# Optimization experiments

Measured on AMD Instinct MI355X. Metric: run time of the kernel, lower is better.

Reference implementation:

```python
import jax, jax.numpy as jnp
import numpy as np

# dims
B, A, CIN, CC = 512, 256, 7, 16          # batch, num_actions, input channels, conv channels
D, H, DH, E = 48, 8, 6, 512              # token_dimension, heads, head_dim, num_embeddings
S, T = 32, 32                            # num_input_tokens, num_output_tokens
AH = H * DH                              # 48
NL = 4                                   # attention layers
CONV_IN = A * CC                         # 4096
ENC = S * D                              # 1536
DEC_OUT = A * CIN                        # 1792
SCALE = float(np.sqrt(D))                # module uses sqrt(input_embedding_dim)
EPS = 1e-5


def _ln(x, g, b):
    m = jnp.mean(x, axis=-1, keepdims=True)
    v = jnp.var(x, axis=-1, keepdims=True)
    return (x - m) * jax.lax.rsqrt(v + EPS) * g + b


def setup_inputs() -> dict:
    key = jax.random.key(0)
    ks = iter(jax.random.split(key, 64))
    def rn(shape, s=0.05):
        return jax.random.normal(next(ks), shape, dtype=jnp.float32) * s
    inp = {}
    inp['x'] = jax.random.normal(next(ks), (B, A, CIN), dtype=jnp.float32)
    inp['u'] = jax.random.uniform(next(ks), (T, B), dtype=jnp.float32)
    inp['bn_g'] = jnp.ones((CIN,), jnp.float32); inp['bn_b'] = jnp.zeros((CIN,), jnp.float32)
    inp['conv_w'] = rn((CC, CIN, 5)); inp['conv_b'] = jnp.zeros((CC,), jnp.float32)
    inp['tk_W1'] = rn((CONV_IN, 2 * CONV_IN)); inp['tk_b1'] = jnp.zeros((2 * CONV_IN,), jnp.float32)
    inp['tk_W2'] = rn((2 * CONV_IN, ENC)); inp['tk_b2'] = jnp.zeros((ENC,), jnp.float32)
    for nm in ('q', 'k', 'v'):
        inp['ln%s_g' % nm] = jnp.ones((NL, D), jnp.float32)
        inp['ln%s_b' % nm] = jnp.zeros((NL, D), jnp.float32)
        inp['W%s' % nm] = rn((NL, D, AH))
        inp['b%s' % nm] = jnp.zeros((NL, AH), jnp.float32)
    inp['Wo'] = rn((NL, AH, D)); inp['bo'] = jnp.zeros((NL, D), jnp.float32)
    inp['mln_g'] = jnp.ones((NL, D), jnp.float32); inp['mln_b'] = jnp.zeros((NL, D), jnp.float32)
    inp['W1'] = rn((NL, D, 2 * D)); inp['b1'] = jnp.zeros((NL, 2 * D), jnp.float32)
    inp['W2'] = rn((NL, 2 * D, D)); inp['b2'] = jnp.zeros((NL, D), jnp.float32)
    inp['emb'] = rn((D, E), 1.0)          # nn.Parameter(torch.randn(D, E))
    inp['pos_enc'] = rn((T, D), 1.0)      # nn.Parameter(torch.randn(T, D))
    inp['dec_W1'] = rn((ENC, 2 * ENC)); inp['dec_b1'] = jnp.zeros((2 * ENC,), jnp.float32)
    inp['dec_W2'] = rn((2 * ENC, DEC_OUT)); inp['dec_b2'] = jnp.zeros((DEC_OUT,), jnp.float32)
    return inp


def _fwd(x, u, bn_g, bn_b, conv_w, conv_b, tk_W1, tk_b1, tk_W2, tk_b2,
         lnq_g, lnq_b, Wq, bq, lnk_g, lnk_b, Wk, bk, lnv_g, lnv_b, Wv, bv, Wo, bo,
         mln_g, mln_b, W1, b1, W2, b2, emb, pos_enc, dec_W1, dec_b1, dec_W2, dec_b2):
    # --- conv stem (BatchNorm1d in training mode: batch statistics) ---
    xt = x.transpose(0, 2, 1)                              # [B, 7, A]
    mu = jnp.mean(xt, axis=(0, 2), keepdims=True)
    var = jnp.var(xt, axis=(0, 2), keepdims=True)
    xn = (xt - mu) * jax.lax.rsqrt(var + EPS) * bn_g[None, :, None] + bn_b[None, :, None]
    xc = jax.lax.conv_general_dilated(xn, conv_w, (1,), ((2, 2),),
                                      dimension_numbers=('NCH', 'OIH', 'NCH')) + conv_b[None, :, None]
    xf = xc.reshape(B, -1)                                 # [B, 16*A]
    h = jax.nn.relu(xf @ tk_W1 + tk_b1)
    toks = (h @ tk_W2 + tk_b2).reshape(B, S, D)            # [B, S, D]

    STOT = S + T
    kc = jnp.zeros((NL, B, H, STOT, DH), jnp.float32)
    vc = jnp.zeros_like(kc)

    # --- prefill pass (output discarded; fills KV caches) ---
    ii = jnp.arange(S)[:, None]; jj = jnp.arange(S)[None, :]
    pre_mask = jnp.where(jj - ii >= S - 1, -999.0, 0.0)    # triu(-999, diagonal=S-1), as in source
    xcur = toks
    for l in range(NL):
        q = (_ln(xcur, lnq_g[l], lnq_b[l]) @ Wq[l] + bq[l]).reshape(B, S, H, DH).transpose(0, 2, 1, 3)
        k = (_ln(xcur, lnk_g[l], lnk_b[l]) @ Wk[l] + bk[l]).reshape(B, S, H, DH).transpose(0, 2, 1, 3)
        v = (_ln(xcur, lnv_g[l], lnv_b[l]) @ Wv[l] + bv[l]).reshape(B, S, H, DH).transpose(0, 2, 1, 3)
        kc = kc.at[l, :, :, :S].set(k)
        vc = vc.at[l, :, :, :S].set(v)
        attn = jax.nn.softmax(jnp.einsum('bhqd,bhkd->bhqk', q, k) / SCALE + pre_mask, axis=-1)
        o = jnp.einsum('bhqk,bhkd->bhqd', attn, v).transpose(0, 2, 1, 3).reshape(B, S, AH)
        xcur = o @ Wo[l] + bo[l] + xcur
        hh = jax.nn.relu(_ln(xcur, mln_g[l], mln_b[l]) @ W1[l] + b1[l])
        xcur = hh @ W2[l] + b2[l]

    jidx = jnp.arange(STOT)

    def step(carry, xs):
        kc, vc = carry
        i, pe, uu = xs
        p = S + i                                          # cache length before this step
        xtk = jnp.broadcast_to(pe, (B, 1, D))
        newk, newv = [], []
        for l in range(NL):
            q = (_ln(xtk, lnq_g[l], lnq_b[l]) @ Wq[l] + bq[l]).reshape(B, 1, H, DH).transpose(0, 2, 1, 3)
            k = (_ln(xtk, lnk_g[l], lnk_b[l]) @ Wk[l] + bk[l]).reshape(B, 1, H, DH).transpose(0, 2, 1, 3)
            v = (_ln(xtk, lnv_g[l], lnv_b[l]) @ Wv[l] + bv[l]).reshape(B, 1, H, DH).transpose(0, 2, 1, 3)
            kcl = jax.lax.dynamic_update_slice(kc[l], k, (0, 0, p, 0))
            vcl = jax.lax.dynamic_update_slice(vc[l], v, (0, 0, p, 0))
            scores = jnp.einsum('bhqd,bhkd->bhqk', q, kcl) / SCALE
            # source mask: -999 added for positions >= mask_offset (includes the new token itself)
            scores = scores + jnp.where(jidx >= p, -999.0, 0.0)
            attn = jax.nn.softmax(scores, axis=-1)
            o = jnp.einsum('bhqk,bhkd->bhqd', attn, vcl).transpose(0, 2, 1, 3).reshape(B, 1, AH)
            xtk = o @ Wo[l] + bo[l] + xtk
            hh = jax.nn.relu(_ln(xtk, mln_g[l], mln_b[l]) @ W1[l] + b1[l])
            xtk = hh @ W2[l] + b2[l]
            newk.append(kcl); newv.append(vcl)
        attended = xtk                                     # [B, 1, D]
        probs = jax.nn.softmax((attended @ emb).reshape(B, E), axis=1)
        cdf = jnp.cumsum(probs, axis=1)
        idx = jnp.clip(jnp.sum((cdf < uu[:, None]).astype(jnp.int32), axis=1), 0, E - 1)
        sel = emb.T[idx].reshape(B, 1, D)
        st = sel + attended - jax.lax.stop_gradient(attended)  # straight-through
        return (jnp.stack(newk), jnp.stack(newv)), st

    (_, _), outs = jax.lax.scan(step, (kc, vc), (jnp.arange(T), pos_enc, u))
    out_tokens = outs.transpose(1, 0, 2, 3).reshape(B, T * D)
    dh_ = jax.nn.relu(out_tokens @ dec_W1 + dec_b1)
    traj = (dh_ @ dec_W2 + dec_b2).reshape(B, A, CIN)
    return traj


def reference(x, u, bn_g, bn_b, conv_w, conv_b, tk_W1, tk_b1, tk_W2, tk_b2,
              lnq_g, lnq_b, Wq, bq, lnk_g, lnk_b, Wk, bk, lnv_g, lnv_b, Wv, bv, Wo, bo,
              mln_g, mln_b, W1, b1, W2, b2, emb, pos_enc, dec_W1, dec_b1, dec_W2, dec_b2):
    return _fwd(x, u, bn_g, bn_b, conv_w, conv_b, tk_W1, tk_b1, tk_W2, tk_b2,
                lnq_g, lnq_b, Wq, bq, lnk_g, lnk_b, Wk, bk, lnv_g, lnv_b, Wv, bv, Wo, bo,
                mln_g, mln_b, W1, b1, W2, b2, emb, pos_enc, dec_W1, dec_b1, dec_W2, dec_b2)
```

## Files before the change

### kernel.cpp

```cpp
#include <hip/hip_runtime.h>

static const double SCALE_ = 6.928203230275509;

__device__ inline float  fma_t(float a, float b, float c)  { return fmaf(a, b, c); }
__device__ inline double fma_t(double a, double b, double c){ return fma(a, b, c); }

__device__ __attribute__((noinline)) double dotW(const double* a,
                                                 const float* W, int n, int ldw,
                                                 double init) {
  double a0 = init, a1 = 0.0;
#pragma unroll 2
  for (int i = 0; i < n; i += 2) {
    a0 = fma(a[i],     (double)W[i * ldw],       a0);
    a1 = fma(a[i + 1], (double)W[(i + 1) * ldw], a1);
  }
  return a0 + a1;
}

template <int N, typename WP>
__device__ __forceinline__ double dotN(const double* a, WP W, int ldw, double init) {
  double c0 = init, c1 = 0.0, c2 = 0.0, c3 = 0.0;
#pragma unroll
  for (int i = 0; i < N; i += 4) {
    c0 = fma(a[i],     (double)W[i * ldw],       c0);
    c1 = fma(a[i + 1], (double)W[(i + 1) * ldw], c1);
    c2 = fma(a[i + 2], (double)W[(i + 2) * ldw], c2);
    c3 = fma(a[i + 3], (double)W[(i + 3) * ldw], c3);
  }
  return (c0 + c1) + (c2 + c3);
}

__device__ __forceinline__ double dot48_row(const double* a, const float* Wrow, double init) {
  double c0 = init, c1 = 0.0, c2 = 0.0, c3 = 0.0;
#pragma unroll
  for (int i = 0; i < 48; i += 4) {
    const float4 wv = *(const float4*)(Wrow + i);
    c0 = fma(a[i],     (double)wv.x, c0);
    c1 = fma(a[i + 1], (double)wv.y, c1);
    c2 = fma(a[i + 2], (double)wv.z, c2);
    c3 = fma(a[i + 3], (double)wv.w, c3);
  }
  return (c0 + c1) + (c2 + c3);
}

__device__ __forceinline__ double dot96_row(const double* a, const float* Wrow, double init) {
  double c0 = init, c1 = 0.0, c2 = 0.0, c3 = 0.0;
#pragma unroll
  for (int i = 0; i < 96; i += 4) {
    const float4 wv = *(const float4*)(Wrow + i);
    c0 = fma(a[i],     (double)wv.x, c0);
    c1 = fma(a[i + 1], (double)wv.y, c1);
    c2 = fma(a[i + 2], (double)wv.z, c2);
    c3 = fma(a[i + 3], (double)wv.w, c3);
  }
  return (c0 + c1) + (c2 + c3);
}

__device__ __attribute__((noinline)) double2 ln_stats48(const double* x) {
  double s0 = 0, s1 = 0, q0 = 0, q1 = 0;
#pragma unroll 2
  for (int i = 0; i < 48; i += 2) {
    const double va = x[i], vb = x[i + 1];
    s0 += va; q0 = fma(va, va, q0);
    s1 += vb; q1 = fma(vb, vb, q1);
  }
  const double m = (s0 + s1) / 48.0;
  const double rs = 1.0 / sqrt((q0 + q1) / 48.0 - m * m + 1e-5);
  return make_double2(m, rs);
}

__device__ __attribute__((noinline)) double exp_ni(double x) { return exp(x); }

__global__ __launch_bounds__(256) void bn_partial_kernel(const float* __restrict__ x,
                                                         double* __restrict__ part) {
  __shared__ double sh[256 * 14];
  const int tid = threadIdx.x;
  const int idx = blockIdx.x * 256 + tid;
  const float* p = x + (size_t)idx * 7;
  for (int c = 0; c < 7; ++c) {
    double v = (double)p[c];
    sh[tid * 14 + c] = v;
    sh[tid * 14 + 7 + c] = v * v;
  }
  __syncthreads();
  if (tid < 14) {
    double acc = 0.0;
    for (int t = 0; t < 256; ++t) acc += sh[t * 14 + tid];
    part[blockIdx.x * 14 + tid] = acc;
  }
}

__global__ void bn_final_kernel(const double* __restrict__ part,
                                const float* __restrict__ g, const float* __restrict__ bb,
                                double* __restrict__ stat) {
  const int c = threadIdx.x;
  if (c < 7) {
    double s = 0.0, s2 = 0.0;
    for (int i = 0; i < 512; ++i) { s += part[i * 14 + c]; s2 += part[i * 14 + 7 + c]; }
    const double mean = s / 131072.0;
    const double var = s2 / 131072.0 - mean * mean;
    const double rstd = 1.0 / sqrt(var + 1e-5);
    const double scale = rstd * (double)g[c];
    stat[c] = scale;
    stat[7 + c] = (double)bb[c] - mean * scale;
  }
}

__global__ __launch_bounds__(256) void conv_kernel(const float* __restrict__ x,
                                                   const float* __restrict__ wconv,
                                                   const float* __restrict__ cb,
                                                   const double* __restrict__ stat,
                                                   double* __restrict__ xf) {
  __shared__ double wsh[560 + 14];
  const int tid = threadIdx.x;
  for (int i = tid; i < 560; i += 256) wsh[i] = (double)wconv[i];
  for (int i = tid; i < 14; i += 256) wsh[560 + i] = stat[i];
  __syncthreads();
  const int idx = blockIdx.x * 256 + tid;
  const int a = idx & 255;
  const int o = (idx >> 8) & 15;
  const int b = idx >> 12;
  double acc = (double)cb[o];
  const float* xb = x + (size_t)b * (256 * 7);
  for (int k = 0; k < 5; ++k) {
    const int pos = a + k - 2;
    if (pos < 0 || pos >= 256) continue;
    const float* xp = xb + pos * 7;
    for (int ci = 0; ci < 7; ++ci) {
      const double xn = (double)xp[ci] * wsh[560 + ci] + wsh[567 + ci];
      acc = fma(xn, wsh[(o * 7 + ci) * 5 + k], acc);
    }
  }
  xf[idx] = acc;
}

template <typename T, bool BIAS, bool RELU>
__global__ __launch_bounds__(256) void gemm128_kernel(const T* __restrict__ A,
                                                      const float* __restrict__ Bm,
                                                      const float* __restrict__ bias,
                                                      T* __restrict__ C,
                                                      const int M, const int N, const int K,
                                                      const int kc) {
  __shared__ T As[16][130];
  __shared__ T Bs[16][66];
  const int tid = threadIdx.x;
  const int tx = tid & 15, ty = tid >> 4;
  const int n0 = blockIdx.x * 64, m0 = blockIdx.y * 128;
  const int k0 = blockIdx.z * kc, kend = k0 + kc;
  const int ar = tid >> 1, ac = (tid & 1) * 8;
  const int br = tid >> 4, bc = (tid & 15) * 4;
  const T* Ap = A + (size_t)(m0 + ar) * K;
  const float* Bp = Bm + (size_t)br * N + n0 + bc;
  T acc[8][4] = {};
  for (int k = k0; k < kend; k += 16) {
    T av8[8];
#pragma unroll
    for (int i = 0; i < 8; ++i) av8[i] = Ap[k + ac + i];
    const float4 bw = *(const float4*)(Bp + (size_t)k * N);
#pragma unroll
    for (int i = 0; i < 8; ++i) As[ac + i][ar] = av8[i];
    Bs[br][bc] = (T)bw.x; Bs[br][bc + 1] = (T)bw.y;
    Bs[br][bc + 2] = (T)bw.z; Bs[br][bc + 3] = (T)bw.w;
    __syncthreads();
#pragma unroll
    for (int kk = 0; kk < 16; ++kk) {
      T a[8], b[4];
#pragma unroll
      for (int i = 0; i < 8; ++i) a[i] = As[kk][ty * 8 + i];
#pragma unroll
      for (int j = 0; j < 4; ++j) b[j] = Bs[kk][tx * 4 + j];
#pragma unroll
      for (int i = 0; i < 8; ++i)
#pragma unroll
        for (int j = 0; j < 4; ++j) acc[i][j] = fma_t(a[i], b[j], acc[i][j]);
    }
    __syncthreads();
  }
  T* Cp = C + (size_t)blockIdx.z * M * N;
#pragma unroll
  for (int i = 0; i < 8; ++i) {
    const int row = m0 + ty * 8 + i;
#pragma unroll
    for (int j = 0; j < 4; ++j) {
      const int col = n0 + tx * 4 + j;
      T v = acc[i][j];
      if (BIAS) v += (T)bias[col];
      if (RELU) v = v > (T)0 ? v : (T)0;
      Cp[(size_t)row * N + col] = v;
    }
  }
}

template <typename T, bool BIAS, bool RELU>
__global__ __launch_bounds__(256) void gemm_kernel(const T* __restrict__ A,
                                                   const float* __restrict__ Bm,
                                                   const float* __restrict__ bias,
                                                   T* __restrict__ C,
                                                   const int M, const int N, const int K,
                                                   const int kc) {
  __shared__ T As[16][65];
  __shared__ T Bs[16][65];
  const int tid = threadIdx.x;
  const int tx = tid & 15, ty = tid >> 4;
  const int n0 = blockIdx.x * 64, m0 = blockIdx.y * 64;
  const int k0 = blockIdx.z * kc, kend = k0 + kc;
  const int ar = tid >> 2, ac = (tid & 3) * 4;
  const int br = tid >> 4, bc = (tid & 15) * 4;
  const T* Ap = A + (size_t)(m0 + ar) * K;
  const float* Bp = Bm + (size_t)br * N + n0 + bc;
  T acc[4][4] = {};
  for (int k = k0; k < kend; k += 16) {
    const T a0 = Ap[k + ac], a1 = Ap[k + ac + 1], a2 = Ap[k + ac + 2], a3 = Ap[k + ac + 3];
    const float4 bw = *(const float4*)(Bp + (size_t)k * N);
    As[ac][ar] = a0; As[ac + 1][ar] = a1; As[ac + 2][ar] = a2; As[ac + 3][ar] = a3;
    Bs[br][bc] = (T)bw.x; Bs[br][bc + 1] = (T)bw.y; Bs[br][bc + 2] = (T)bw.z; Bs[br][bc + 3] = (T)bw.w;
    __syncthreads();
#pragma unroll
    for (int kk = 0; kk < 16; ++kk) {
      T av[4], bv2[4];
#pragma unroll
      for (int i = 0; i < 4; ++i) av[i] = As[kk][ty * 4 + i];
#pragma unroll
      for (int j = 0; j < 4; ++j) bv2[j] = Bs[kk][tx * 4 + j];
#pragma unroll
      for (int i = 0; i < 4; ++i)
#pragma unroll
        for (int j = 0; j < 4; ++j) acc[i][j] = fma_t(av[i], bv2[j], acc[i][j]);
    }
    __syncthreads();
  }
  T* Cp = C + (size_t)blockIdx.z * M * N;
#pragma unroll
  for (int i = 0; i < 4; ++i) {
    const int row = m0 + ty * 4 + i;
#pragma unroll
    for (int j = 0; j < 4; ++j) {
      const int col = n0 + tx * 4 + j;
      T v = acc[i][j];
      if (BIAS) v += (T)bias[col];
      if (RELU) v = v > (T)0 ? v : (T)0;
      Cp[(size_t)row * N + col] = v;
    }
  }
}

__global__ __launch_bounds__(256) void reduce2_bias_kernel(const double* __restrict__ part,
                                                           const float* __restrict__ bias,
                                                           double* __restrict__ out,
                                                           const int MN, const int N) {
  const int i = blockIdx.x * 256 + threadIdx.x;
  if (i < MN) out[i] = part[i] + part[MN + i] + (double)bias[i % N];
}

__global__ __launch_bounds__(256) void transpose_weights_kernel(
    const float* __restrict__ Wq, const float* __restrict__ Wk,
    const float* __restrict__ Wv, const float* __restrict__ Wo,
    const float* __restrict__ W1, const float* __restrict__ W2,
    const float* __restrict__ emb,
    float* __restrict__ WqT, float* __restrict__ WkT,
    float* __restrict__ WvT, float* __restrict__ WoT,
    float* __restrict__ W1T, float* __restrict__ W2T,
    float* __restrict__ embT) {
  const int t = blockIdx.x * 256 + threadIdx.x;
  if (t < 36864) {
    const int a = t / 9216, r = t - a * 9216;
    const int l = r / 2304, e = r - l * 2304;
    const int i = e / 48, j = e - i * 48;
    const float* src = a == 0 ? Wq : a == 1 ? Wk : a == 2 ? Wv : Wo;
    float* dst = a == 0 ? WqT : a == 1 ? WkT : a == 2 ? WvT : WoT;
    dst[l * 2304 + j * 48 + i] = src[l * 2304 + i * 48 + j];
  } else if (t < 55296) {
    const int t1 = t - 36864;
    const int l = t1 / 4608, e = t1 - l * 4608;
    const int i = e / 96, j = e - i * 96;
    W1T[l * 4608 + j * 48 + i] = W1[l * 4608 + i * 96 + j];
  } else if (t < 73728) {
    const int t2 = t - 55296;
    const int l = t2 / 4608, e = t2 - l * 4608;
    const int i = e / 48, j = e - i * 48;
    W2T[l * 4608 + j * 96 + i] = W2[l * 4608 + i * 48 + j];
  } else {
    const int t3 = t - 73728;
    const int d = t3 / 512, e = t3 - d * 512;
    embT[e * 48 + d] = emb[d * 512 + e];
  }
}

__global__ __launch_bounds__(256) void prefill_kernel(
    const double* __restrict__ toks,
    const float* __restrict__ lnq_g, const float* __restrict__ lnq_b,
    const float* __restrict__ Wq, const float* __restrict__ bq,
    const float* __restrict__ lnk_g, const float* __restrict__ lnk_b,
    const float* __restrict__ Wk, const float* __restrict__ bk,
    const float* __restrict__ lnv_g, const float* __restrict__ lnv_b,
    const float* __restrict__ Wv, const float* __restrict__ bvv,
    const float* __restrict__ Wo, const float* __restrict__ bo,
    const float* __restrict__ mln_g, const float* __restrict__ mln_b,
    const float* __restrict__ W1, const float* __restrict__ b1,
    const float* __restrict__ W2, const float* __restrict__ b2,
    float* __restrict__ kc32, float* __restrict__ vc32) {
  const int b = blockIdx.x, tid = threadIdx.x;
  __shared__ double xcur[1536], abuf[1536], qbuf[1536], kvbuf[3072];
  __shared__ double mean[32], rstd[32];
  double* kb = kvbuf;
  double* vb = kvbuf + 1536;

#pragma unroll 1
  for (int i = tid; i < 1536; i += 256) xcur[i] = toks[(size_t)b * 1536 + i];
  __syncthreads();

#pragma unroll 1
  for (int l = 0; l < 4; ++l) {
    if (tid < 32) {
      double s = 0.0, s2 = 0.0;
#pragma unroll 4
      for (int i = 0; i < 48; ++i) { const double v = xcur[tid * 48 + i]; s += v; s2 += v * v; }
      const double m = s / 48.0;
      mean[tid] = m;
      rstd[tid] = 1.0 / sqrt(s2 / 48.0 - m * m + 1e-5);
    }
    __syncthreads();
    const bool last = (l == 3);

    if (!last) {
#pragma unroll 1
      for (int i = tid; i < 1536; i += 256) {
        const int t = i / 48, d = i % 48;
        abuf[i] = (xcur[i] - mean[t]) * rstd[t] * (double)lnq_g[l * 48 + d] + (double)lnq_b[l * 48 + d];
      }
      __syncthreads();
#pragma unroll 1
      for (int i = tid; i < 1536; i += 256) {
        const int t = i / 48, j = i % 48;
        qbuf[i] = dotW(abuf + t * 48, Wq + l * 2304 + j, 48, 48, (double)bq[l * 48 + j]);
      }
      __syncthreads();
    }
#pragma unroll 1
    for (int i = tid; i < 1536; i += 256) {
      const int t = i / 48, d = i % 48;
      abuf[i] = (xcur[i] - mean[t]) * rstd[t] * (double)lnk_g[l * 48 + d] + (double)lnk_b[l * 48 + d];
    }
    __syncthreads();
#pragma unroll 1
    for (int i = tid; i < 1536; i += 256) {
      const int t = i / 48, j = i % 48;
      kb[i] = dotW(abuf + t * 48, Wk + l * 2304 + j, 48, 48, (double)bk[l * 48 + j]);
    }
    __syncthreads();
#pragma unroll 1
    for (int i = tid; i < 1536; i += 256) {
      const int t = i / 48, d = i % 48;
      abuf[i] = (xcur[i] - mean[t]) * rstd[t] * (double)lnv_g[l * 48 + d] + (double)lnv_b[l * 48 + d];
    }
    __syncthreads();
#pragma unroll 1
    for (int i = tid; i < 1536; i += 256) {
      const int t = i / 48, j = i % 48;
      vb[i] = dotW(abuf + t * 48, Wv + l * 2304 + j, 48, 48, (double)bvv[l * 48 + j]);
    }
    __syncthreads();
#pragma unroll 1
    for (int i = tid; i < 1536; i += 256) {
      const int t = i / 48, j = i % 48;
      const int h = j / 6, d = j % 6;
      const size_t ci = ((((size_t)b * 4 + l) * 8 + h) * 32 + t) * 6 + d;
      kc32[ci] = (float)kb[i];
      vc32[ci] = (float)vb[i];
    }

    if (!last) {
      const int t = tid >> 3, h = tid & 7;
      const double* qp = qbuf + t * 48 + h * 6;
      const double q0 = qp[0], q1 = qp[1], q2 = qp[2], q3 = qp[3], q4 = qp[4], q5 = qp[5];
      double mx = -1e300;
#pragma unroll 4
      for (int j = 0; j < 32; ++j) {
        const double* kp = kb + j * 48 + h * 6;
        double sv = q0 * kp[0];
        sv = fma(q1, kp[1], sv); sv = fma(q2, kp[2], sv); sv = fma(q3, kp[3], sv);
        sv = fma(q4, kp[4], sv); sv = fma(q5, kp[5], sv);
        sv /= SCALE_;
        if (t == 0 && j == 31) sv -= 999.0;
        mx = sv > mx ? sv : mx;
      }
      double den = 0, o0 = 0, o1 = 0, o2 = 0, o3 = 0, o4 = 0, o5 = 0;
#pragma unroll 4
      for (int j = 0; j < 32; ++j) {
        const double* kp = kb + j * 48 + h * 6;
        double sv = q0 * kp[0];
        sv = fma(q1, kp[1], sv); sv = fma(q2, kp[2], sv); sv = fma(q3, kp[3], sv);
        sv = fma(q4, kp[4], sv); sv = fma(q5, kp[5], sv);
        sv /= SCALE_;
        if (t == 0 && j == 31) sv -= 999.0;
        const double e = exp_ni(sv - mx);
        den += e;
        const double* vp = vb + j * 48 + h * 6;
        o0 = fma(e, vp[0], o0); o1 = fma(e, vp[1], o1); o2 = fma(e, vp[2], o2);
        o3 = fma(e, vp[3], o3); o4 = fma(e, vp[4], o4); o5 = fma(e, vp[5], o5);
      }
      abuf[t * 48 + h * 6 + 0] = o0 / den;
      abuf[t * 48 + h * 6 + 1] = o1 / den;
      abuf[t * 48 + h * 6 + 2] = o2 / den;
      abuf[t * 48 + h * 6 + 3] = o3 / den;
      abuf[t * 48 + h * 6 + 4] = o4 / den;
      abuf[t * 48 + h * 6 + 5] = o5 / den;
      __syncthreads();
#pragma unroll 1
      for (int i = tid; i < 1536; i += 256) {
        const int t2 = i / 48, j = i % 48;
        xcur[i] += dotW(abuf + t2 * 48, Wo + l * 2304 + j, 48, 48, (double)bo[l * 48 + j]);
      }
      __syncthreads();
      if (tid < 32) {
        double s = 0.0, s2 = 0.0;
#pragma unroll 4
        for (int i = 0; i < 48; ++i) { const double v = xcur[tid * 48 + i]; s += v; s2 += v * v; }
        const double m = s / 48.0;
        mean[tid] = m;
        rstd[tid] = 1.0 / sqrt(s2 / 48.0 - m * m + 1e-5);
      }
      __syncthreads();
#pragma unroll 1
      for (int i = tid; i < 1536; i += 256) {
        const int t2 = i / 48, d = i % 48;
        qbuf[i] = (xcur[i] - mean[t2]) * rstd[t2] * (double)mln_g[l * 48 + d] + (double)mln_b[l * 48 + d];
      }
      __syncthreads();
#pragma unroll 1
      for (int i = tid; i < 3072; i += 256) {
        const int t2 = i / 96, jj = i % 96;
        const double acc = dotW(qbuf + t2 * 48, W1 + l * 4608 + jj, 48, 96, (double)b1[l * 96 + jj]);
        kvbuf[i] = acc > 0 ? acc : 0;
      }
      __syncthreads();
#pragma unroll 1
      for (int i = tid; i < 1536; i += 256) {
        const int t2 = i / 48, j = i % 48;
        abuf[i] = dotW(kvbuf + t2 * 96, W2 + l * 4608 + j, 96, 48, (double)b2[l * 48 + j]);
      }
      __syncthreads();
#pragma unroll 1
      for (int i = tid; i < 1536; i += 256) xcur[i] = abuf[i];
      __syncthreads();
    }
  }
}

__global__ __launch_bounds__(256, 2) void ar_kernel(
    const float* __restrict__ pos_enc, const float* __restrict__ u,
    const float* __restrict__ lnq_g, const float* __restrict__ lnq_b,
    const float* __restrict__ WqT, const float* __restrict__ bq,
    const float* __restrict__ lnk_g, const float* __restrict__ lnk_b,
    const float* __restrict__ WkT, const float* __restrict__ bk,
    const float* __restrict__ lnv_g, const float* __restrict__ lnv_b,
    const float* __restrict__ WvT, const float* __restrict__ bvv,
    const float* __restrict__ WoT, const float* __restrict__ bo,
    const float* __restrict__ mln_g, const float* __restrict__ mln_b,
    const float* __restrict__ W1T, const float* __restrict__ b1,
    const float* __restrict__ W2T, const float* __restrict__ b2,
    const float* __restrict__ emb,
    const float* __restrict__ kc32, const float* __restrict__ vc32,
    float* __restrict__ out_tok) {
  const int b = blockIdx.x, tid = threadIdx.x;
  __shared__ float knew[4][8][32][7];
  __shared__ float vnew[4][8][32][7];
  __shared__ double xtk[48], anorm[144], qs[48], os[48], hh[96];
  __shared__ double probs[512], red[4];
  __shared__ float par[2880];
  {
    const float* srcs[14] = {lnq_g, lnq_b, lnk_g, lnk_b, lnv_g, lnv_b, mln_g, mln_b,
                             bq, bk, bvv, bo, b1, b2};
    const int sz[14] = {192, 192, 192, 192, 192, 192, 192, 192, 192, 192, 192, 192, 384, 192};
    int base = 0;
#pragma unroll 1
    for (int a2 = 0; a2 < 14; ++a2) {
      for (int i = tid; i < sz[a2]; i += 256) par[base + i] = srcs[a2][i];
      base += sz[a2];
    }
  }
  __syncthreads();

  const int hl = tid >> 5, rl = tid & 31;

#pragma unroll 1
  for (int step = 0; step < 32; ++step) {
    const int p = 32 + step;
    if (tid < 48) xtk[tid] = (double)pos_enc[step * 48 + tid];
    __syncthreads();

#pragma unroll 1
    for (int l = 0; l < 4; ++l) {
      {
        const double2 st = ln_stats48(xtk);
        if (tid < 144) {
          const int which = tid / 48, d = tid - which * 48;
          const float* gp = par + 384 * which;
          const float* bp = gp + 192;
          anorm[tid] = (xtk[d] - st.x) * st.y * (double)gp[l * 48 + d] + (double)bp[l * 48 + d];
        }
      }
      __syncthreads();
      if (tid < 144) {
        const int which = tid / 48, j = tid - which * 48;
        const float* WT = which == 0 ? WqT : which == 1 ? WkT : WvT;
        const float* bbp = par + 1536 + 192 * which;
        const double acc = dot48_row(anorm + which * 48, WT + l * 2304 + j * 48,
                                     (double)bbp[l * 48 + j]);
        if (which == 0) {
          qs[j] = acc;
        } else {
          const int h2 = j / 6, d2 = j - h2 * 6;
          if (which == 1) knew[l][h2][step][d2] = (float)acc;
          else            vnew[l][h2][step][d2] = (float)acc;
        }
      }
      __syncthreads();
      {
        const size_t gb = (((size_t)b * 4 + l) * 8 + hl) * 192 + rl * 6;
        const float* kg = kc32 + gb;
        const float* vg = vc32 + gb;
        const double qv0 = qs[hl * 6 + 0], qv1 = qs[hl * 6 + 1], qv2 = qs[hl * 6 + 2],
                     qv3 = qs[hl * 6 + 3], qv4 = qs[hl * 6 + 4], qv5 = qs[hl * 6 + 5];
        const bool has2 = rl < step;
        double sv1 = qv0 * (double)kg[0];
        sv1 = fma(qv1, (double)kg[1], sv1); sv1 = fma(qv2, (double)kg[2], sv1);
        sv1 = fma(qv3, (double)kg[3], sv1); sv1 = fma(qv4, (double)kg[4], sv1);
        sv1 = fma(qv5, (double)kg[5], sv1);
        sv1 /= SCALE_;
        double sv2 = -1e300;
        if (has2) {
          const float* kh = &knew[l][hl][rl][0];
          double t2 = qv0 * (double)kh[0];
          t2 = fma(qv1, (double)kh[1], t2); t2 = fma(qv2, (double)kh[2], t2);
          t2 = fma(qv3, (double)kh[3], t2); t2 = fma(qv4, (double)kh[4], t2);
          t2 = fma(qv5, (double)kh[5], t2);
          sv2 = t2 / SCALE_;
        }
        double mx = sv1 > sv2 ? sv1 : sv2;
#pragma unroll
        for (int off = 1; off < 32; off <<= 1) { const double o2 = __shfl_xor(mx, off); mx = o2 > mx ? o2 : mx; }
        const double e1 = exp(sv1 - mx);
        const double e2 = has2 ? exp(sv2 - mx) : 0.0;
        double den = e1 + e2;
        double o[6];
#pragma unroll
        for (int d = 0; d < 6; ++d) o[d] = e1 * (double)vg[d];
        if (has2) {
          const float* vh = &vnew[l][hl][rl][0];
#pragma unroll
          for (int d = 0; d < 6; ++d) o[d] = fma(e2, (double)vh[d], o[d]);
        }
#pragma unroll
        for (int off = 1; off < 32; off <<= 1) {
          den += __shfl_xor(den, off);
#pragma unroll
          for (int d = 0; d < 6; ++d) o[d] += __shfl_xor(o[d], off);
        }
        if (rl == 0) {
#pragma unroll
          for (int d = 0; d < 6; ++d) os[hl * 6 + d] = o[d] / den;
        }
      }
      __syncthreads();
      if (tid < 48)
        xtk[tid] += dot48_row(os, WoT + l * 2304 + tid * 48, (double)par[2112 + l * 48 + tid]);
      __syncthreads();
      {
        const double2 st = ln_stats48(xtk);
        if (tid < 48)
          anorm[tid] = (xtk[tid] - st.x) * st.y * (double)par[1152 + l * 48 + tid]
                       + (double)par[1344 + l * 48 + tid];
      }
      __syncthreads();
      if (tid < 96) {
        const double v2 = dot48_row(anorm, W1T + l * 4608 + tid * 48, (double)par[2304 + l * 96 + tid]);
        hh[tid] = v2 > 0 ? v2 : 0;
      }
      __syncthreads();
      if (tid < 48)
        xtk[tid] = dot96_row(hh, W2T + l * 4608 + tid * 96, (double)par[2688 + l * 48 + tid]);
      __syncthreads();
    }

    {
      const double lg1 = dotN<48>(xtk, emb + tid, 512, 0.0);
      const double lg2 = dotN<48>(xtk, emb + 256 + tid, 512, 0.0);
      double mx = lg1 > lg2 ? lg1 : lg2;
#pragma unroll
      for (int off = 1; off < 64; off <<= 1) { const double o2 = __shfl_xor(mx, off); mx = o2 > mx ? o2 : mx; }
      if ((tid & 63) == 0) red[tid >> 6] = mx;
      __syncthreads();
      {
        const double m0 = red[0] > red[1] ? red[0] : red[1];
        const double m1 = red[2] > red[3] ? red[2] : red[3];
        mx = m0 > m1 ? m0 : m1;
      }
      probs[tid] = exp(lg1 - mx);
      probs[tid + 256] = exp(lg2 - mx);
      __syncthreads();
      if (tid < 64) {
        const int lane = tid;
        double loc[8], run = 0;
#pragma unroll
        for (int n2 = 0; n2 < 8; ++n2) { run += probs[lane * 8 + n2]; loc[n2] = run; }
        double incl = run;
#pragma unroll
        for (int off = 1; off < 64; off <<= 1) {
          const double t2 = __shfl_up(incl, off);
          if (lane >= off) incl += t2;
        }
        const double excl = incl - run;
        const double Ssum = __shfl(incl, 63);
        const double uu = (double)u[step * 512 + b];
        int cnt = 0;
#pragma unroll
        for (int n2 = 0; n2 < 8; ++n2) cnt += ((excl + loc[n2]) / Ssum < uu) ? 1 : 0;
#pragma unroll
        for (int off = 1; off < 64; off <<= 1) cnt += __shfl_xor(cnt, off);
        const int idx = cnt > 511 ? 511 : cnt;
        if (lane < 48) {
          const double sel = (double)emb[lane * 512 + idx];
          const double att = xtk[lane];
          out_tok[(size_t)b * 1536 + step * 48 + lane] = (float)((sel + att) - att);
        }
      }
      __syncthreads();
    }
  }
}

extern "C" void kernel_launch(void* const* d_in, const int* in_sizes, int n_in,
                              void* d_out, int out_size, void* d_ws, size_t ws_size,
                              hipStream_t stream) {
  const float* x      = (const float*)d_in[0];
  const float* u      = (const float*)d_in[1];
  const float* bn_g   = (const float*)d_in[2];
  const float* bn_b   = (const float*)d_in[3];
  const float* conv_w = (const float*)d_in[4];
  const float* conv_b = (const float*)d_in[5];
  const float* tk_W1  = (const float*)d_in[6];
  const float* tk_b1  = (const float*)d_in[7];
  const float* tk_W2  = (const float*)d_in[8];
  const float* tk_b2  = (const float*)d_in[9];
  const float* lnq_g  = (const float*)d_in[10];
  const float* lnq_b  = (const float*)d_in[11];
  const float* Wq     = (const float*)d_in[12];
  const float* bq     = (const float*)d_in[13];
  const float* lnk_g  = (const float*)d_in[14];
  const float* lnk_b  = (const float*)d_in[15];
  const float* Wk     = (const float*)d_in[16];
  const float* bk     = (const float*)d_in[17];
  const float* lnv_g  = (const float*)d_in[18];
  const float* lnv_b  = (const float*)d_in[19];
  const float* Wv     = (const float*)d_in[20];
  const float* bvv    = (const float*)d_in[21];
  const float* Wo     = (const float*)d_in[22];
  const float* bo     = (const float*)d_in[23];
  const float* mln_g  = (const float*)d_in[24];
  const float* mln_b  = (const float*)d_in[25];
  const float* W1     = (const float*)d_in[26];
  const float* b1     = (const float*)d_in[27];
  const float* W2     = (const float*)d_in[28];
  const float* b2     = (const float*)d_in[29];
  const float* emb    = (const float*)d_in[30];
  const float* pos    = (const float*)d_in[31];
  const float* dW1    = (const float*)d_in[32];
  const float* db1    = (const float*)d_in[33];
  const float* dW2    = (const float*)d_in[34];
  const float* db2    = (const float*)d_in[35];
  float* out = (float*)d_out;

  char* w = (char*)d_ws;
  size_t off = 0;
  auto alloc = [&](size_t bytes) {
    size_t o = off;
    off = (off + bytes + 255) & ~(size_t)255;
    return o;
  };
  const size_t o_bnp  = alloc(512 * 14 * 8);
  const size_t o_bns  = alloc(14 * 8);
  const size_t o_xf   = alloc(16777216);
  const size_t o_h    = alloc(33554432);
  const size_t o_toks = alloc(6291456);
  const size_t o_kc   = alloc(12582912);
  const size_t o_vc   = alloc(12582912);

  double* bnp  = (double*)(w + o_bnp);
  double* bns  = (double*)(w + o_bns);
  double* xf   = (double*)(w + o_xf);
  double* hbuf = (double*)(w + o_h);
  double* toks = (double*)(w + o_toks);
  float*  kc32 = (float*)(w + o_kc);
  float*  vc32 = (float*)(w + o_vc);
  double* part = (double*)(w + o_xf);
  float*  otok = (float*)(w + o_h);
  float*  dh   = (float*)(w + o_h + 4194304);
  float* WqT  = (float*)(w + o_h + 16777216);
  float* WkT  = WqT + 9216;
  float* WvT  = WkT + 9216;
  float* WoT  = WvT + 9216;
  float* W1T  = WoT + 9216;
  float* W2T  = W1T + 18432;
  float* embT = W2T + 18432;

  bn_partial_kernel<<<512, 256, 0, stream>>>(x, bnp);
  bn_final_kernel<<<1, 64, 0, stream>>>(bnp, bn_g, bn_b, bns);
  conv_kernel<<<8192, 256, 0, stream>>>(x, conv_w, conv_b, bns, xf);
  gemm128_kernel<double, true, true><<<dim3(128, 4, 1), 256, 0, stream>>>(
      xf, tk_W1, tk_b1, hbuf, 512, 8192, 4096, 4096);
  gemm128_kernel<double, false, false><<<dim3(24, 4, 2), 256, 0, stream>>>(
      hbuf, tk_W2, nullptr, part, 512, 1536, 8192, 4096);
  reduce2_bias_kernel<<<3072, 256, 0, stream>>>(part, tk_b2, toks, 512 * 1536, 1536);
  transpose_weights_kernel<<<384, 256, 0, stream>>>(Wq, Wk, Wv, Wo, W1, W2, emb,
      WqT, WkT, WvT, WoT, W1T, W2T, embT);
  prefill_kernel<<<512, 256, 0, stream>>>(toks,
      lnq_g, lnq_b, Wq, bq, lnk_g, lnk_b, Wk, bk, lnv_g, lnv_b, Wv, bvv,
      Wo, bo, mln_g, mln_b, W1, b1, W2, b2, kc32, vc32);
  ar_kernel<<<512, 256, 0, stream>>>(pos, u,
      lnq_g, lnq_b, WqT, bq, lnk_g, lnk_b, WkT, bk, lnv_g, lnv_b, WvT, bvv,
      WoT, bo, mln_g, mln_b, W1T, b1, W2T, b2, emb, kc32, vc32, otok);
  gemm_kernel<float, true, true><<<dim3(48, 8, 1), 256, 0, stream>>>(
      otok, dW1, db1, dh, 512, 3072, 1536, 1536);
  gemm_kernel<float, true, false><<<dim3(28, 8, 1), 256, 0, stream>>>(
      dh, dW2, db2, out, 512, 1792, 3072, 3072);
}
```

Measured before the change: 4.462 ms.

## Prefetch weights into registers, fuse layernorm stats via wave shuffles, lighten barriers

The sequential decode kernel now loads the Q/K/V, Wo and W1 weight rows and the K/V cache values into registers before the barriers that precede their use. The idea is to overlap global load latency with earlier phases. Layernorm statistics are computed once per wave with shuffle reductions and broadcast through shared memory, replacing the per-thread serial ln_stats48 loops. This fuses the Wo projection, residual add and layernorm into one phase and removes a barrier. __syncthreads is replaced by a custom barrier that waits only on LDS counters, which relies on register-held global loads not needing a vmcnt wait and raises register pressure.

Result: slower. 4.803 ms (+7.6%).

```diff
diff --git a/kernel.cpp b/kernel.cpp
--- a/kernel.cpp
+++ b/kernel.cpp
@@ -4,6 +4,12 @@
 
 __device__ inline float  fma_t(float a, float b, float c)  { return fmaf(a, b, c); }
 __device__ inline double fma_t(double a, double b, double c){ return fma(a, b, c); }
+
+#define BARRIER() do {                                         \
+    asm volatile("s_waitcnt lgkmcnt(0)" ::: "memory");         \
+    __builtin_amdgcn_s_barrier();                              \
+    asm volatile("" ::: "memory");                             \
+  } while (0)
 
 __device__ __attribute__((noinline)) double dotW(const double* a,
                                                  const float* W, int n, int ldw,
@@ -54,19 +60,6 @@
     c3 = fma(a[i + 3], (double)wv.w, c3);
   }
   return (c0 + c1) + (c2 + c3);
-}
-
-__device__ __attribute__((noinline)) double2 ln_stats48(const double* x) {
-  double s0 = 0, s1 = 0, q0 = 0, q1 = 0;
-#pragma unroll 2
-  for (int i = 0; i < 48; i += 2) {
-    const double va = x[i], vb = x[i + 1];
-    s0 += va; q0 = fma(va, va, q0);
-    s1 += vb; q1 = fma(vb, vb, q1);
-  }
-  const double m = (s0 + s1) / 48.0;
-  const double rs = 1.0 / sqrt((q0 + q1) / 48.0 - m * m + 1e-5);
-  return make_double2(m, rs);
 }
 
 __device__ __attribute__((noinline)) double exp_ni(double x) { return exp(x); }
@@ -467,6 +460,7 @@
   __shared__ float vnew[4][8][32][7];
   __shared__ double xtk[48], anorm[144], qs[48], os[48], hh[96];
   __shared__ double probs[512], red[4];
+  __shared__ double smean, srstd;
   __shared__ float par[2880];
   {
     const float* srcs[14] = {lnq_g, lnq_b, lnk_g, lnk_b, lnv_g, lnv_b, mln_g, mln_b,
@@ -479,54 +473,85 @@
       base += sz[a2];
     }
   }
-  __syncthreads();
+  BARRIER();
 
   const int hl = tid >> 5, rl = tid & 31;
+  const int which = tid < 144 ? tid / 48 : 0;
+  const int jj = tid < 144 ? tid - which * 48 : 0;
 
 #pragma unroll 1
   for (int step = 0; step < 32; ++step) {
-    const int p = 32 + step;
-    if (tid < 48) xtk[tid] = (double)pos_enc[step * 48 + tid];
-    __syncthreads();
+    if (tid < 64) {
+      double xv = 0.0;
+      if (tid < 48) xv = (double)pos_enc[step * 48 + tid];
+      double s = tid < 48 ? xv : 0.0;
+      double q = tid < 48 ? xv * xv : 0.0;
+#pragma unroll
+      for (int off = 1; off < 64; off <<= 1) { s += __shfl_xor(s, off); q += __shfl_xor(q, off); }
+      const double m = s / 48.0;
+      const double rs = 1.0 / sqrt(q / 48.0 - m * m + 1e-5);
+      if (tid < 48) xtk[tid] = xv;
+      if (tid == 0) { smean = m; srstd = rs; }
+    }
+    BARRIER();
 
 #pragma unroll 1
     for (int l = 0; l < 4; ++l) {
+      float kgr[6], vgr[6];
       {
-        const double2 st = ln_stats48(xtk);
-        if (tid < 144) {
-          const int which = tid / 48, d = tid - which * 48;
-          const float* gp = par + 384 * which;
-          const float* bp = gp + 192;
-          anorm[tid] = (xtk[d] - st.x) * st.y * (double)gp[l * 48 + d] + (double)bp[l * 48 + d];
-        }
-      }
-      __syncthreads();
+        const float* kg = kc32 + (size_t)b * 6144 + l * 1536 + hl * 192 + rl * 6;
+        const float* vg = vc32 + (size_t)b * 6144 + l * 1536 + hl * 192 + rl * 6;
+#pragma unroll
+        for (int d = 0; d < 6; ++d) { kgr[d] = kg[d]; vgr[d] = vg[d]; }
+      }
+      float4 wr[12];
       if (tid < 144) {
-        const int which = tid / 48, j = tid - which * 48;
         const float* WT = which == 0 ? WqT : which == 1 ? WkT : WvT;
+        const float4* wp = (const float4*)(WT + l * 2304 + jj * 48);
+#pragma unroll
+        for (int q2 = 0; q2 < 12; ++q2) wr[q2] = wp[q2];
+        const double m = smean, rs = srstd;
+        const float* gp = par + 384 * which;
+        const float* bp = gp + 192;
+        anorm[tid] = (xtk[jj] - m) * rs * (double)gp[l * 48 + jj] + (double)bp[l * 48 + jj];
+      }
+      BARRIER();
+      if (tid < 144) {
         const float* bbp = par + 1536 + 192 * which;
-        const double acc = dot48_row(anorm + which * 48, WT + l * 2304 + j * 48,
-                                     (double)bbp[l * 48 + j]);
+        double c0 = (double)bbp[l * 48 + jj], c1 = 0.0, c2 = 0.0, c3 = 0.0;
+        const double* a = anorm + which * 48;
+#pragma unroll
+        for (int i = 0; i < 48; i += 4) {
+          const float4 wv = wr[i >> 2];
+          c0 = fma(a[i],     (double)wv.x, c0);
+          c1 = fma(a[i + 1], (double)wv.y, c1);
+          c2 = fma(a[i + 2], (double)wv.z, c2);
+          c3 = fma(a[i + 3], (double)wv.w, c3);
+        }
+        const double acc = (c0 + c1) + (c2 + c3);
         if (which == 0) {
-          qs[j] = acc;
+          qs[jj] = acc;
         } else {
-          const int h2 = j / 6, d2 = j - h2 * 6;
+          const int h2 = jj / 6, d2 = jj - h2 * 6;
           if (which == 1) knew[l][h2][step][d2] = (float)acc;
           else            vnew[l][h2][step][d2] = (float)acc;
         }
       }
-      __syncthreads();
+      BARRIER();
+      float4 wo[12];
+      if (tid < 48) {
+        const float4* wp = (const float4*)(WoT + l * 2304 + tid * 48);
+#pragma unroll
+        for (int q2 = 0; q2 < 12; ++q2) wo[q2] = wp[q2];
+      }
       {
-        const size_t gb = (((size_t)b * 4 + l) * 8 + hl) * 192 + rl * 6;
-        const float* kg = kc32 + gb;
-        const float* vg = vc32 + gb;
         const double qv0 = qs[hl * 6 + 0], qv1 = qs[hl * 6 + 1], qv2 = qs[hl * 6 + 2],
                      qv3 = qs[hl * 6 + 3], qv4 = qs[hl * 6 + 4], qv5 = qs[hl * 6 + 5];
         const bool has2 = rl < step;
-        double sv1 = qv0 * (double)kg[0];
-        sv1 = fma(qv1, (double)kg[1], sv1); sv1 = fma(qv2, (double)kg[2], sv1);
-        sv1 = fma(qv3, (double)kg[3], sv1); sv1 = fma(qv4, (double)kg[4], sv1);
-        sv1 = fma(qv5, (double)kg[5], sv1);
+        double sv1 = qv0 * (double)kgr[0];
+        sv1 = fma(qv1, (double)kgr[1], sv1); sv1 = fma(qv2, (double)kgr[2], sv1);
+        sv1 = fma(qv3, (double)kgr[3], sv1); sv1 = fma(qv4, (double)kgr[4], sv1);
+        sv1 = fma(qv5, (double)kgr[5], sv1);
         sv1 /= SCALE_;
         double sv2 = -1e300;
         if (has2) {
@@ -545,7 +570,7 @@
         double den = e1 + e2;
         double o[6];
 #pragma unroll
-        for (int d = 0; d < 6; ++d) o[d] = e1 * (double)vg[d];
+        for (int d = 0; d < 6; ++d) o[d] = e1 * (double)vgr[d];
         if (has2) {
           const float* vh = &vnew[l][hl][rl][0];
 #pragma unroll
@@ -562,25 +587,68 @@
           for (int d = 0; d < 6; ++d) os[hl * 6 + d] = o[d] / den;
         }
       }
-      __syncthreads();
-      if (tid < 48)
-        xtk[tid] += dot48_row(os, WoT + l * 2304 + tid * 48, (double)par[2112 + l * 48 + tid]);
-      __syncthreads();
-      {
-        const double2 st = ln_stats48(xtk);
+      BARRIER();
+      float4 w1r[12];
+      if (tid < 96) {
+        const float4* wp = (const float4*)(W1T + l * 4608 + tid * 48);
+#pragma unroll
+        for (int q2 = 0; q2 < 12; ++q2) w1r[q2] = wp[q2];
+      }
+      if (tid < 64) {
+        double xv = 0.0;
+        if (tid < 48) {
+          double c0 = (double)par[2112 + l * 48 + tid], c1 = 0.0, c2 = 0.0, c3 = 0.0;
+#pragma unroll
+          for (int i = 0; i < 48; i += 4) {
+            const float4 wv = wo[i >> 2];
+            c0 = fma(os[i],     (double)wv.x, c0);
+            c1 = fma(os[i + 1], (double)wv.y, c1);
+            c2 = fma(os[i + 2], (double)wv.z, c2);
+            c3 = fma(os[i + 3], (double)wv.w, c3);
+          }
+          xv = xtk[tid] + ((c0 + c1) + (c2 + c3));
+        }
+        double s = tid < 48 ? xv : 0.0;
+        double q = tid < 48 ? xv * xv : 0.0;
+#pragma unroll
+        for (int off = 1; off < 64; off <<= 1) { s += __shfl_xor(s, off); q += __shfl_xor(q, off); }
+        const double m = s / 48.0;
+        const double rs = 1.0 / sqrt(q / 48.0 - m * m + 1e-5);
+        if (tid < 48) {
+          xtk[tid] = xv;
+          anorm[tid] = (xv - m) * rs * (double)par[1152 + l * 48 + tid]
+                       + (double)par[1344 + l * 48 + tid];
+        }
+      }
+      BARRIER();
+      if (tid < 96) {
+        double c0 = (double)par[2304 + l * 96 + tid], c1 = 0.0, c2 = 0.0, c3 = 0.0;
+#pragma unroll
+        for (int i = 0; i < 48; i += 4) {
+          const float4 wv = w1r[i >> 2];
+          c0 = fma(anorm[i],     (double)wv.x, c0);
+          c1 = fma(anorm[i + 1], (double)wv.y, c1);
+          c2 = fma(anorm[i + 2], (double)wv.z, c2);
+          c3 = fma(anorm[i + 3], (double)wv.w, c3);
+        }
+        const double v2 = (c0 + c1) + (c2 + c3);
+        hh[tid] = v2 > 0 ? v2 : 0;
+      }
+      BARRIER();
+      if (tid < 64) {
+        double xv = 0.0;
         if (tid < 48)
-          anorm[tid] = (xtk[tid] - st.x) * st.y * (double)par[1152 + l * 48 + tid]
-                       + (double)par[1344 + l * 48 + tid];
-      }
-      __syncthreads();
-      if (tid < 96) {
-        const double v2 = dot48_row(anorm, W1T + l * 4608 + tid * 48, (double)par[2304 + l * 96 + tid]);
-        hh[tid] = v2 > 0 ? v2 : 0;
-      }
-      __syncthreads();
-      if (tid < 48)
-        xtk[tid] = dot96_row(hh, W2T + l * 4608 + tid * 96, (double)par[2688 + l * 48 + tid]);
-      __syncthreads();
+          xv = dot96_row(hh, W2T + l * 4608 + tid * 96, (double)par[2688 + l * 48 + tid]);
+        double s = tid < 48 ? xv : 0.0;
+        double q = tid < 48 ? xv * xv : 0.0;
+#pragma unroll
+        for (int off = 1; off < 64; off <<= 1) { s += __shfl_xor(s, off); q += __shfl_xor(q, off); }
+        const double m = s / 48.0;
+        const double rs = 1.0 / sqrt(q / 48.0 - m * m + 1e-5);
+        if (tid < 48) xtk[tid] = xv;
+        if (tid == 0) { smean = m; srstd = rs; }
+      }
+      BARRIER();
     }
 
     {
@@ -590,7 +658,7 @@
 #pragma unroll
       for (int off = 1; off < 64; off <<= 1) { const double o2 = __shfl_xor(mx, off); mx = o2 > mx ? o2 : mx; }
       if ((tid & 63) == 0) red[tid >> 6] = mx;
-      __syncthreads();
+      BARRIER();
       {
         const double m0 = red[0] > red[1] ? red[0] : red[1];
         const double m1 = red[2] > red[3] ? red[2] : red[3];
@@ -598,7 +666,7 @@
       }
       probs[tid] = exp(lg1 - mx);
       probs[tid + 256] = exp(lg2 - mx);
-      __syncthreads();
+      BARRIER();
       if (tid < 64) {
         const int lane = tid;
         double loc[8], run = 0;
@@ -625,7 +693,7 @@
           out_tok[(size_t)b * 1536 + step * 48 + lane] = (float)((sel + att) - att);
         }
       }
-      __syncthreads();
+      BARRIER();
     }
   }
 }
```
